# Kernel optimization log

Measured on AMD Instinct MI355X. Metric: run time of the kernel, lower is better.

Reference implementation:

```python
import jax, jax.numpy as jnp
import numpy as np

V, N = 3, 32768
C2, C3 = 256, 32          # feat_ch_2D, feat_ch_3D
H = W = 128               # 2D feature map size
D = 32                    # 3D volume feature size
CIN = C2 + C3             # 288, MLP in_channels


def setup_inputs() -> dict:
    key = jax.random.key(0)
    ks = jax.random.split(key, 16)
    sc = 0.02
    inp = {
        'pts': jax.random.uniform(ks[0], (1, N, 3), minval=-0.5, maxval=0.5),
        'pts_proj': jax.random.uniform(ks[1], (1, N, 2), minval=-1.0, maxval=1.0),
        'img_feat0': jax.random.normal(ks[2], (V, C2, H, W)),
        'img_feat1': jax.random.normal(ks[3], (V, C2, H, W)),
        'vol_feat0': jax.random.normal(ks[4], (V, C3, D, D, D)),
        'vol_feat1': jax.random.normal(ks[5], (V, C3, D, D, D)),
        'W0': jax.random.normal(ks[6], (1024, CIN)) * sc,  'b0': jnp.zeros((1024,)),
        'W1': jax.random.normal(ks[7], (512, CIN + 1024)) * sc, 'b1': jnp.zeros((512,)),
        'W2': jax.random.normal(ks[8], (256, CIN + 512)) * sc,  'b2': jnp.zeros((256,)),
        'W3': jax.random.normal(ks[9], (128, CIN + 256)) * sc,  'b3': jnp.zeros((128,)),
        'W4': jax.random.normal(ks[10], (1, 128)) * sc,         'b4': jnp.zeros((1,)),
        'mean_num': 3,
    }
    return inp


def _gs2d(feat, gx, gy):
    # feat: [C,H,W]; gx,gy: [N] normalized coords in [-1,1]
    C, Hh, Ww = feat.shape
    ix = jnp.clip(((gx + 1.0) * Ww - 1.0) * 0.5, 0.0, Ww - 1.0)  # align_corners=False, border pad
    iy = jnp.clip(((gy + 1.0) * Hh - 1.0) * 0.5, 0.0, Hh - 1.0)
    x0f, y0f = jnp.floor(ix), jnp.floor(iy)
    wx, wy = ix - x0f, iy - y0f
    x0 = x0f.astype(jnp.int32); x1 = jnp.minimum(x0 + 1, Ww - 1)
    y0 = y0f.astype(jnp.int32); y1 = jnp.minimum(y0 + 1, Hh - 1)
    v00 = feat[:, y0, x0]; v01 = feat[:, y0, x1]
    v10 = feat[:, y1, x0]; v11 = feat[:, y1, x1]
    return (v00 * (1 - wy) * (1 - wx) + v01 * (1 - wy) * wx
            + v10 * wy * (1 - wx) + v11 * wy * wx)  # [C,N]


def _gs3d(feat, gx, gy, gz):
    # feat: [C,D,H,W]; grid x->W, y->H, z->D (torch grid_sample convention)
    C, Dd, Hh, Ww = feat.shape
    ix = jnp.clip(((gx + 1.0) * Ww - 1.0) * 0.5, 0.0, Ww - 1.0)
    iy = jnp.clip(((gy + 1.0) * Hh - 1.0) * 0.5, 0.0, Hh - 1.0)
    iz = jnp.clip(((gz + 1.0) * Dd - 1.0) * 0.5, 0.0, Dd - 1.0)
    x0f, y0f, z0f = jnp.floor(ix), jnp.floor(iy), jnp.floor(iz)
    wx, wy, wz = ix - x0f, iy - y0f, iz - z0f
    x0 = x0f.astype(jnp.int32); x1 = jnp.minimum(x0 + 1, Ww - 1)
    y0 = y0f.astype(jnp.int32); y1 = jnp.minimum(y0 + 1, Hh - 1)
    z0 = z0f.astype(jnp.int32); z1 = jnp.minimum(z0 + 1, Dd - 1)
    def g(zi, yi, xi):
        return feat[:, zi, yi, xi]  # [C,N]
    out = (g(z0, y0, x0) * (1 - wz) * (1 - wy) * (1 - wx)
           + g(z0, y0, x1) * (1 - wz) * (1 - wy) * wx
           + g(z0, y1, x0) * (1 - wz) * wy * (1 - wx)
           + g(z0, y1, x1) * (1 - wz) * wy * wx
           + g(z1, y0, x0) * wz * (1 - wy) * (1 - wx)
           + g(z1, y0, x1) * wz * (1 - wy) * wx
           + g(z1, y1, x0) * wz * wy * (1 - wx)
           + g(z1, y1, x1) * wz * wy * wx)
    return out  # [C,N]


def _lrelu(x):
    return jnp.where(x >= 0, x, 0.2 * x)


def _conv1x1(Wm, bm, x):
    # x: [V,C,N] -> [V,O,N]
    return jnp.einsum('oc,vcn->von', Wm, x) + bm[None, :, None]


def _mlp0(x, W0, b0, W1, b1, W2, b2, W3, b3):
    out = _lrelu(_conv1x1(W0, b0, x))
    out = _lrelu(_conv1x1(W1, b1, jnp.concatenate([x, out], axis=1)))
    out = _lrelu(_conv1x1(W2, b2, jnp.concatenate([x, out], axis=1)))
    out = _lrelu(_conv1x1(W3, b3, jnp.concatenate([x, out], axis=1)))
    return out  # [V,128,N]


def _forward(pts, pts_proj, img_feats, vol_feats,
             W0, b0, W1, b1, W2, b2, W3, b3, W4, b4, mean_num):
    v = img_feats[0].shape[0]
    gx2 = jnp.broadcast_to(pts_proj[:, :, 0], (v, pts_proj.shape[1]))
    gy2 = jnp.broadcast_to(pts_proj[:, :, 1], (v, pts_proj.shape[1]))
    p = pts * 2.0  # pts *= 2.0 before 3D sampling
    gx3 = jnp.broadcast_to(p[:, :, 0], (v, p.shape[1]))
    gy3 = jnp.broadcast_to(p[:, :, 1], (v, p.shape[1]))
    gz3 = jnp.broadcast_to(p[:, :, 2], (v, p.shape[1]))
    outs = []
    for img_feat, vol_feat in zip(img_feats, vol_feats):
        f2 = jax.vmap(_gs2d)(img_feat, gx2, gy2)            # [V,C2,N]
        f3 = jax.vmap(_gs3d)(vol_feat, gx3, gy3, gz3)       # [V,C3,N]
        pt_feat = jnp.concatenate([f2, f3], axis=1)         # [V,288,N]
        pt_out0 = _mlp0(pt_feat, W0, b0, W1, b1, W2, b2, W3, b3)
        pt_out0_mean = jnp.mean(pt_out0[:mean_num], axis=0, keepdims=True)  # [1,128,N]
        sdf = jax.nn.sigmoid(_conv1x1(W4, b4, pt_out0_mean))                # [1,1,N]
        outs.append(jnp.transpose(sdf, (0, 2, 1)))                          # [1,N,1]
    return tuple(outs)


def reference(pts, pts_proj, img_feat0, img_feat1, vol_feat0, vol_feat1,
              W0, b0, W1, b1, W2, b2, W3, b3, W4, b4, mean_num):
    return _forward(pts, pts_proj, [img_feat0, img_feat1], [vol_feat0, vol_feat1],
                    W0, b0, W1, b1, W2, b2, W3, b3, W4, b4, mean_num)
```

## Files before the change

### kernel.cpp

```cpp
#include <hip/hip_runtime.h>
#include <hip/hip_bf16.h>

#define NV 3
#define NPTS 32768
#define C2C 256
#define C3C 32
#define CINC 288
#define CINP 320
#define HH 128
#define WWW 128
#define DDD 32

typedef short bh8 __attribute__((ext_vector_type(8)));
typedef float fx4 __attribute__((ext_vector_type(4)));
typedef unsigned short us4 __attribute__((ext_vector_type(4)));

__device__ __forceinline__ float b2f(unsigned short u) {
    unsigned int x = ((unsigned int)u) << 16;
    return __uint_as_float(x);
}
__device__ __forceinline__ unsigned short f2b(float f) {
    unsigned int x = __float_as_uint(f);
    unsigned int r = (x + 0x7FFFu + ((x >> 16) & 1u)) >> 16;
    return (unsigned short)r;
}

__device__ __forceinline__ void gl2lds16(const unsigned short* g, unsigned short* l) {
    __builtin_amdgcn_global_load_lds(
        (const __attribute__((address_space(1))) unsigned int*)g,
        (__attribute__((address_space(3))) unsigned int*)l, 16, 0, 0);
}

__device__ __forceinline__ int xcd_swz(int orig, int nwg) {
    int xcd = orig & 7;
    int q = nwg >> 3, r = nwg & 7;
    int base = (xcd < r) ? xcd * (q + 1) : r * (q + 1) + (xcd - r) * q;
    return base + (orig >> 3);
}

__global__ void k_wpad(const float* __restrict__ src, unsigned short* __restrict__ dst, int M, int Kp) {
    int idx = blockIdx.x * 256 + threadIdx.x;
    if (idx >= M * Kp) return;
    int m = idx / Kp, k = idx - m * Kp;
    int Ksrc = Kp - 32;
    float v;
    if (k < CINC) v = src[(size_t)m * Ksrc + k];
    else if (k < CINP) v = 0.0f;
    else v = src[(size_t)m * Ksrc + (k - 32)];
    dst[idx] = f2b(v);
}

__global__ void k_timg(const float* __restrict__ in, unsigned short* __restrict__ out) {
    int v = blockIdx.x >> 7, y = blockIdx.x & 127;
    int x0 = blockIdx.y << 6, c0 = blockIdx.z << 6;
    __shared__ float t[64][65];
    int tx = threadIdx.x & 63, tg = threadIdx.x >> 6;
    const float* src = in + (((size_t)(v * C2C + c0) * HH + y) * WWW + x0);
#pragma unroll
    for (int i = 0; i < 16; i++) {
        int cl = tg * 16 + i;
        t[cl][tx] = src[(size_t)cl * (HH * WWW) + tx];
    }
    __syncthreads();
    unsigned short* dst = out + ((size_t)(v * HH + y) * WWW + x0) * C2C + c0;
#pragma unroll
    for (int i = 0; i < 16; i++) {
        int xl = tg * 16 + i;
        dst[(size_t)xl * C2C + tx] = f2b(t[tx][xl]);
    }
}

__global__ void k_tvol(const float* __restrict__ in, unsigned short* __restrict__ out) {
    int v = blockIdx.x;
    int s0 = blockIdx.y << 8;
    __shared__ float t[32][257];
    int tid = threadIdx.x;
    const float* src = in + (size_t)v * C3C * 32768 + s0;
#pragma unroll
    for (int c = 0; c < 32; c++) t[c][tid] = src[(size_t)c * 32768 + tid];
    __syncthreads();
    unsigned short* dst = out + ((size_t)v * 32768 + s0) * C3C;
    int c = tid & 31, sb = tid >> 5;
#pragma unroll
    for (int j = 0; j < 32; j++) {
        int sl = j * 8 + sb;
        dst[(size_t)sl * C3C + c] = f2b(t[c][sl]);
    }
}

__global__ __launch_bounds__(256) void k_sample(const float* __restrict__ pts, const float* __restrict__ proj,
                         const unsigned short* __restrict__ imgT, const unsigned short* __restrict__ volT,
                         unsigned short* __restrict__ ptT, int n0, int Nk) {
    int w = threadIdx.x >> 6, l = threadIdx.x & 63;
    int i = blockIdx.x * 4 + w;
    int v = blockIdx.y;
    int n = n0 + i;
    unsigned short* dstRow = ptT + (size_t)(v * Nk + i) * CINP;

    {
        float gx = proj[n * 2 + 0], gy = proj[n * 2 + 1];
        float ix = fminf(fmaxf(((gx + 1.0f) * (float)WWW - 1.0f) * 0.5f, 0.0f), (float)(WWW - 1));
        float iy = fminf(fmaxf(((gy + 1.0f) * (float)HH - 1.0f) * 0.5f, 0.0f), (float)(HH - 1));
        float x0f = floorf(ix), y0f = floorf(iy);
        float wx = ix - x0f, wy = iy - y0f;
        int x0 = (int)x0f, y0 = (int)y0f;
        int x1 = min(x0 + 1, WWW - 1), y1 = min(y0 + 1, HH - 1);
        const unsigned short* base = imgT + (size_t)v * HH * WWW * C2C;
        us4 a = *((const us4*)(base + ((size_t)(y0 * WWW + x0)) * C2C) + l);
        us4 b = *((const us4*)(base + ((size_t)(y0 * WWW + x1)) * C2C) + l);
        us4 c = *((const us4*)(base + ((size_t)(y1 * WWW + x0)) * C2C) + l);
        us4 d = *((const us4*)(base + ((size_t)(y1 * WWW + x1)) * C2C) + l);
        float w00 = (1.0f - wy) * (1.0f - wx), w01 = (1.0f - wy) * wx;
        float w10 = wy * (1.0f - wx), w11 = wy * wx;
        us4 rv;
#pragma unroll
        for (int r = 0; r < 4; r++) {
            float f = b2f(a[r]) * w00 + b2f(b[r]) * w01 + b2f(c[r]) * w10 + b2f(d[r]) * w11;
            rv[r] = f2b(f);
        }
        *(us4*)(dstRow + l * 4) = rv;
    }
    {
        float gx = pts[n * 3 + 0] * 2.0f, gy = pts[n * 3 + 1] * 2.0f, gz = pts[n * 3 + 2] * 2.0f;
        float ix = fminf(fmaxf(((gx + 1.0f) * (float)DDD - 1.0f) * 0.5f, 0.0f), (float)(DDD - 1));
        float iy = fminf(fmaxf(((gy + 1.0f) * (float)DDD - 1.0f) * 0.5f, 0.0f), (float)(DDD - 1));
        float iz = fminf(fmaxf(((gz + 1.0f) * (float)DDD - 1.0f) * 0.5f, 0.0f), (float)(DDD - 1));
        float x0f = floorf(ix), y0f = floorf(iy), z0f = floorf(iz);
        float wx = ix - x0f, wy = iy - y0f, wz = iz - z0f;
        int x0 = (int)x0f, y0 = (int)y0f, z0 = (int)z0f;
        int x1 = min(x0 + 1, DDD - 1), y1 = min(y0 + 1, DDD - 1), z1 = min(z0 + 1, DDD - 1);
        int c = l & 31, zs = l >> 5;
        int zi = zs ? z1 : z0;
        float wzs = zs ? wz : (1.0f - wz);
        const unsigned short* base = volT + (size_t)v * 32768 * C3C;
        float f00 = b2f(base[((size_t)((zi * 32 + y0) * 32 + x0)) * C3C + c]);
        float f01 = b2f(base[((size_t)((zi * 32 + y0) * 32 + x1)) * C3C + c]);
        float f10 = b2f(base[((size_t)((zi * 32 + y1) * 32 + x0)) * C3C + c]);
        float f11 = b2f(base[((size_t)((zi * 32 + y1) * 32 + x1)) * C3C + c]);
        float r = (f00 * (1.0f - wy) * (1.0f - wx) + f01 * (1.0f - wy) * wx +
                   f10 * wy * (1.0f - wx) + f11 * wy * wx) * wzs;
        float other = __shfl_xor(r, 32);
        r += other;
        if (zs == 0) dstRow[C2C + c] = f2b(r);
    }
    if (l < 8) *(us4*)(dstRow + CINC + l * 4) = (us4){0, 0, 0, 0};
}

__global__ __launch_bounds__(512) void k_gemm8(const unsigned short* __restrict__ A, int Kp,
                                               const unsigned short* __restrict__ B1,
                                               const unsigned short* __restrict__ B2, int K2,
                                               const float* __restrict__ bias,
                                               unsigned short* __restrict__ C, int M) {
    __shared__ unsigned short As[2][256 * 64];
    __shared__ unsigned short Bs[2][256 * 64];
    int tid = threadIdx.x;
    int w = tid >> 6, l = tid & 63;
    int la = l & 15, lg = l >> 4;
    int wm = w >> 2, wn = w & 3;
    int g = wn >> 1;
    int gx = gridDim.x;
    int nwg = gx * gridDim.y;
    int bid = xcd_swz(blockIdx.y * gx + blockIdx.x, nwg);
    int mBlk = (bid % gx) * 256;
    int nBlk = (bid / gx) * 256;
    int nt = Kp >> 6;

    const unsigned short* Ag = A + (size_t)mBlk * Kp;

    fx4 acc[8][4];
#pragma unroll
    for (int mi = 0; mi < 8; mi++)
#pragma unroll
        for (int ni = 0; ni < 4; ni++) acc[mi][ni] = (fx4){0.f, 0.f, 0.f, 0.f};

    auto burst = [&](int t, int nxt) {
        const unsigned short* bsrc;
        size_t ldb;
        int kc;
        if (t < 5) { bsrc = B1; ldb = CINP; kc = t * 64; }
        else       { bsrc = B2; ldb = (size_t)K2; kc = (t - 5) * 64; }
        bsrc += (size_t)nBlk * ldb + kc;
        const unsigned short* asrc = Ag + t * 64;
#pragma unroll
        for (int h = 0; h < 2; h++)
#pragma unroll
            for (int j = 0; j < 2; j++) {
                int idx = j * 512 + tid;
                int r = (h << 7) + (idx >> 3);
                int c = (idx & 7) ^ (r & 7);
                gl2lds16(asrc + (size_t)r * Kp + c * 8, &As[nxt][(h << 13) + idx * 8]);
            }
#pragma unroll
        for (int h = 0; h < 2; h++)
#pragma unroll
            for (int j = 0; j < 2; j++) {
                int idx = j * 512 + tid;
                int r = (h << 7) + (idx >> 3);
                int c = (idx & 7) ^ (r & 7);
                gl2lds16(bsrc + (size_t)r * ldb + c * 8, &Bs[nxt][(h << 13) + idx * 8]);
            }
    };

    burst(0, 0);
    for (int t = 0; t < nt; t++) {
        int cur = t & 1;
        if (t + 1 < nt) {
            burst(t + 1, cur ^ 1);
            if (g == 0) asm volatile("s_waitcnt vmcnt(10)" ::: "memory");
            else        asm volatile("s_waitcnt vmcnt(8)" ::: "memory");
        } else {
            if (g == 0) asm volatile("s_waitcnt vmcnt(2)" ::: "memory");
            else        asm volatile("s_waitcnt vmcnt(0)" ::: "memory");
        }
        const unsigned short* Ab = &As[cur][0];
        const unsigned short* Bb = &Bs[cur][0];
        bh8 afr[4][2];
#pragma unroll
        for (int p = 0; p < 4; p++) {
            int qm = p >> 1, qn = p & 1;
            if (qn == 0) {
#pragma unroll
                for (int m2 = 0; m2 < 4; m2++)
#pragma unroll
                    for (int s = 0; s < 2; s++) {
                        int row = wm * 128 + (qm * 4 + m2) * 16 + la;
                        int c = (s * 4 + lg) ^ (row & 7);
                        afr[m2][s] = *(const bh8*)&Ab[row * 64 + c * 8];
                    }
            }
            bh8 bfr[2][2];
#pragma unroll
            for (int n2 = 0; n2 < 2; n2++)
#pragma unroll
                for (int s = 0; s < 2; s++) {
                    int row = wn * 64 + (qn * 2 + n2) * 16 + la;
                    int c = (s * 4 + lg) ^ (row & 7);
                    bfr[n2][s] = *(const bh8*)&Bb[row * 64 + c * 8];
                }
            __builtin_amdgcn_s_barrier();
            __builtin_amdgcn_s_setprio(1);
#pragma unroll
            for (int m2 = 0; m2 < 4; m2++)
#pragma unroll
                for (int n2 = 0; n2 < 2; n2++)
#pragma unroll
                    for (int s = 0; s < 2; s++)
                        acc[qm * 4 + m2][qn * 2 + n2] = __builtin_amdgcn_mfma_f32_16x16x32_bf16(
                            afr[m2][s], bfr[n2][s], acc[qm * 4 + m2][qn * 2 + n2], 0, 0, 0);
            __builtin_amdgcn_s_setprio(0);
            if (p == 3) asm volatile("s_waitcnt lgkmcnt(0)" ::: "memory");
            __builtin_amdgcn_s_barrier();
        }
    }

#pragma unroll
    for (int mi = 0; mi < 8; mi++) {
        int m0 = mBlk + wm * 128 + mi * 16 + lg * 4;
        fx4 bb = *(const fx4*)(bias + m0);
#pragma unroll
        for (int ni = 0; ni < 4; ni++) {
            int n = nBlk + wn * 64 + ni * 16 + la;
            us4 rv;
#pragma unroll
            for (int r = 0; r < 4; r++) {
                float x = acc[mi][ni][r] + bb[r];
                x = (x >= 0.0f) ? x : 0.2f * x;
                rv[r] = f2b(x);
            }
            *(us4*)(C + (size_t)n * M + m0) = rv;
        }
    }
}

__global__ __launch_bounds__(256) void k_gemm(const unsigned short* __restrict__ A, int K,
                                              const unsigned short* __restrict__ B1, int K1,
                                              const unsigned short* __restrict__ B2, int K2,
                                              const float* __restrict__ bias,
                                              unsigned short* __restrict__ C, int M) {
    __shared__ unsigned short Ash[128 * 32];
    __shared__ unsigned short Bsh[128 * 32];
    int tid = threadIdx.x;
    int w = tid >> 6, l = tid & 63;
    int la = l & 15, lg = l >> 4;
    int wm = w & 1, wn = w >> 1;
    int gx = gridDim.x;
    int nwg = gx * gridDim.y;
    int bid = xcd_swz(blockIdx.y * gx + blockIdx.x, nwg);
    int mBlk = (bid % gx) * 128;
    int nBlk = (bid / gx) * 128;

    int sRow = l >> 2;
    int sCol = (l & 3) * 8;

    fx4 acc[4][4];
#pragma unroll
    for (int mi = 0; mi < 4; mi++)
#pragma unroll
        for (int ni = 0; ni < 4; ni++) acc[mi][ni] = (fx4){0.f, 0.f, 0.f, 0.f};

    const unsigned short* Ag = A + (size_t)mBlk * K;
    const unsigned short* Bg;

#define KLOOP(BPTR, KB, AOFF)                                                                  \
    Bg = (BPTR) + (size_t)nBlk * (KB);                                                         \
    for (int k0 = 0; k0 < (KB); k0 += 32) {                                                    \
        _Pragma("unroll")                                                                      \
        for (int j = 0; j < 2; j++) {                                                          \
            int r = w * 32 + j * 16 + sRow;                                                    \
            gl2lds16(Ag + (size_t)r * K + (AOFF) + k0 + sCol, &Ash[r * 32 + sCol]);            \
            gl2lds16(Bg + (size_t)r * (KB) + k0 + sCol, &Bsh[r * 32 + sCol]);                  \
        }                                                                                      \
        __syncthreads();                                                                       \
        bh8 af[4], bfv[4];                                                                     \
        _Pragma("unroll")                                                                      \
        for (int mi = 0; mi < 4; mi++) af[mi] = *(const bh8*)&Ash[(wm * 64 + mi * 16 + la) * 32 + lg * 8]; \
        _Pragma("unroll")                                                                      \
        for (int ni = 0; ni < 4; ni++) bfv[ni] = *(const bh8*)&Bsh[(wn * 64 + ni * 16 + la) * 32 + lg * 8]; \
        _Pragma("unroll")                                                                      \
        for (int mi = 0; mi < 4; mi++)                                                         \
            _Pragma("unroll")                                                                  \
            for (int ni = 0; ni < 4; ni++)                                                     \
                acc[mi][ni] = __builtin_amdgcn_mfma_f32_16x16x32_bf16(af[mi], bfv[ni], acc[mi][ni], 0, 0, 0); \
        __syncthreads();                                                                       \
    }

    KLOOP(B1, K1, 0)
    if (B2 != nullptr) {
        KLOOP(B2, K2, K1)
    }
#undef KLOOP

#pragma unroll
    for (int mi = 0; mi < 4; mi++) {
        int m0 = mBlk + wm * 64 + mi * 16 + lg * 4;
        fx4 bb = *(const fx4*)(bias + m0);
#pragma unroll
        for (int ni = 0; ni < 4; ni++) {
            int n = nBlk + wn * 64 + ni * 16 + la;
            us4 rv;
#pragma unroll
            for (int r = 0; r < 4; r++) {
                float x = acc[mi][ni][r] + bb[r];
                x = (x >= 0.0f) ? x : 0.2f * x;
                rv[r] = f2b(x);
            }
            *(us4*)(C + (size_t)n * M + m0) = rv;
        }
    }
}

__global__ void k_head(const unsigned short* __restrict__ o3, const float* __restrict__ W4,
                       const float* __restrict__ b4, const int* __restrict__ mn_p,
                       float* __restrict__ out, int n0, int Nk, int level) {
    int i = blockIdx.x * 256 + threadIdx.x;
    if (i >= Nk) return;
    int mn = *mn_p;
    if (mn > NV) mn = NV;
    if (mn < 1) mn = 1;
    float s = 0.0f;
    for (int v = 0; v < mn; v++) {
        const unsigned short* row = o3 + (size_t)(v * Nk + i) * 128;
        for (int c0 = 0; c0 < 128; c0 += 8) {
            bh8 x = *(const bh8*)(row + c0);
#pragma unroll
            for (int r = 0; r < 8; r++) s += W4[c0 + r] * b2f((unsigned short)x[r]);
        }
    }
    s = s / (float)mn + b4[0];
    out[(size_t)level * NPTS + n0 + i] = 1.0f / (1.0f + expf(-s));
}

extern "C" void kernel_launch(void* const* d_in, const int* in_sizes, int n_in,
                              void* d_out, int out_size, void* d_ws, size_t ws_size,
                              hipStream_t stream) {
    const float* pts = (const float*)d_in[0];
    const float* proj = (const float*)d_in[1];
    const float* img[2] = {(const float*)d_in[2], (const float*)d_in[3]};
    const float* vol[2] = {(const float*)d_in[4], (const float*)d_in[5]};
    const float* Wf[4] = {(const float*)d_in[6], (const float*)d_in[8], (const float*)d_in[10], (const float*)d_in[12]};
    const float* bf[4] = {(const float*)d_in[7], (const float*)d_in[9], (const float*)d_in[11], (const float*)d_in[13]};
    const float* W4 = (const float*)d_in[14];
    const float* b4 = (const float*)d_in[15];
    const int* mn = (const int*)d_in[16];
    float* out = (float*)d_out;

    const int Kp[4] = {320, 1344, 832, 576};
    const int Msz[4] = {1024, 512, 256, 128};

    char* ws = (char*)d_ws;
    size_t off = 0;
    auto alloc = [&](size_t bytes) -> char* {
        char* p = ws + off;
        off = (off + bytes + 255) & ~(size_t)255;
        return p;
    };

    unsigned short* Wb[4];
    for (int i = 0; i < 4; i++) Wb[i] = (unsigned short*)alloc((size_t)Msz[i] * Kp[i] * 2);
    unsigned short* imgT = (unsigned short*)alloc((size_t)NV * HH * WWW * C2C * 2);
    unsigned short* volT = (unsigned short*)alloc((size_t)NV * 32768 * C3C * 2);
    size_t fixed = off;

    const size_t perPt = (size_t)NV * 2 * (CINP + 1024 + 512 + 256 + 128);
    int Nk = NPTS;
    if (fixed + (size_t)Nk * perPt + 4096 > ws_size) {
        size_t avail = (ws_size > fixed + 4096) ? (ws_size - fixed - 4096) : 0;
        long nk = (long)(avail / perPt);
        nk = (nk / 256) * 256;
        if (nk < 256) nk = 256;
        if (nk > NPTS) nk = NPTS;
        Nk = (int)nk;
    }
    unsigned short* ptT = (unsigned short*)alloc((size_t)NV * Nk * CINP * 2);
    unsigned short* o0 = (unsigned short*)alloc((size_t)NV * Nk * 1024 * 2);
    unsigned short* o1 = (unsigned short*)alloc((size_t)NV * Nk * 512 * 2);
    unsigned short* o2 = (unsigned short*)alloc((size_t)NV * Nk * 256 * 2);
    unsigned short* o3 = (unsigned short*)alloc((size_t)NV * Nk * 128 * 2);

    for (int i = 0; i < 4; i++) {
        int n = Msz[i] * Kp[i];
        k_wpad<<<(n + 255) / 256, 256, 0, stream>>>(Wf[i], Wb[i], Msz[i], Kp[i]);
    }

    for (int lvl = 0; lvl < 2; lvl++) {
        k_timg<<<dim3(NV * HH, WWW / 64, C2C / 64), 256, 0, stream>>>(img[lvl], imgT);
        k_tvol<<<dim3(NV, 32768 / 256), 256, 0, stream>>>(vol[lvl], volT);
        for (int n0 = 0; n0 < NPTS; n0 += Nk) {
            int nk = NPTS - n0 < Nk ? NPTS - n0 : Nk;
            int NC = NV * nk;
            k_sample<<<dim3(nk / 4, NV), 256, 0, stream>>>(pts, proj, imgT, volT, ptT, n0, nk);
            k_gemm8<<<dim3(1024 / 256, NC / 256), 512, 0, stream>>>(Wb[0], Kp[0], ptT, nullptr, 0, bf[0], o0, 1024);
            k_gemm8<<<dim3(512 / 256, NC / 256), 512, 0, stream>>>(Wb[1], Kp[1], ptT, o0, 1024, bf[1], o1, 512);
            k_gemm8<<<dim3(256 / 256, NC / 256), 512, 0, stream>>>(Wb[2], Kp[2], ptT, o1, 512, bf[2], o2, 256);
            k_gemm<<<dim3(128 / 128, NC / 128), 256, 0, stream>>>(Wb[3], Kp[3], ptT, CINP, o2, 256, bf[3], o3, 128);
            k_head<<<(nk + 255) / 256, 256, 0, stream>>>(o3, W4, b4, mn, out, n0, nk, lvl);
        }
    }
}
```

Measured before the change: 1.183 ms.

## Batch both feature levels into a single MLP pass and switch layer tile kernels

Transposes both levels' image and volume features up front, then samples and runs the MLP for both levels at once. Each GEMM launch therefore covers twice as many columns, which halves the number of launches and gives more blocks per grid. Layers 0 and 2 also move from the 256-tile k_gemm8 kernel to the 128-tile k_gemm kernel. The cost is double the workspace for activations and a smaller per-chunk point count if the workspace is tight.

Result: slower. 1.233 ms (+4.3%).

```diff
diff --git a/kernel.cpp b/kernel.cpp
--- a/kernel.cpp
+++ b/kernel.cpp
@@ -90,12 +90,14 @@
 
 __global__ __launch_bounds__(256) void k_sample(const float* __restrict__ pts, const float* __restrict__ proj,
                          const unsigned short* __restrict__ imgT, const unsigned short* __restrict__ volT,
+                         size_t imgStride, size_t volStride,
                          unsigned short* __restrict__ ptT, int n0, int Nk) {
     int w = threadIdx.x >> 6, l = threadIdx.x & 63;
     int i = blockIdx.x * 4 + w;
     int v = blockIdx.y;
+    int lvl = blockIdx.z;
     int n = n0 + i;
-    unsigned short* dstRow = ptT + (size_t)(v * Nk + i) * CINP;
+    unsigned short* dstRow = ptT + (size_t)((lvl * NV + v) * Nk + i) * CINP;
 
     {
         float gx = proj[n * 2 + 0], gy = proj[n * 2 + 1];
@@ -105,7 +107,7 @@
         float wx = ix - x0f, wy = iy - y0f;
         int x0 = (int)x0f, y0 = (int)y0f;
         int x1 = min(x0 + 1, WWW - 1), y1 = min(y0 + 1, HH - 1);
-        const unsigned short* base = imgT + (size_t)v * HH * WWW * C2C;
+        const unsigned short* base = imgT + lvl * imgStride + (size_t)v * HH * WWW * C2C;
         us4 a = *((const us4*)(base + ((size_t)(y0 * WWW + x0)) * C2C) + l);
         us4 b = *((const us4*)(base + ((size_t)(y0 * WWW + x1)) * C2C) + l);
         us4 c = *((const us4*)(base + ((size_t)(y1 * WWW + x0)) * C2C) + l);
@@ -132,7 +134,7 @@
         int c = l & 31, zs = l >> 5;
         int zi = zs ? z1 : z0;
         float wzs = zs ? wz : (1.0f - wz);
-        const unsigned short* base = volT + (size_t)v * 32768 * C3C;
+        const unsigned short* base = volT + lvl * volStride + (size_t)v * 32768 * C3C;
         float f00 = b2f(base[((size_t)((zi * 32 + y0) * 32 + x0)) * C3C + c]);
         float f01 = b2f(base[((size_t)((zi * 32 + y0) * 32 + x1)) * C3C + c]);
         float f10 = b2f(base[((size_t)((zi * 32 + y1) * 32 + x0)) * C3C + c]);
@@ -351,15 +353,16 @@
 
 __global__ void k_head(const unsigned short* __restrict__ o3, const float* __restrict__ W4,
                        const float* __restrict__ b4, const int* __restrict__ mn_p,
-                       float* __restrict__ out, int n0, int Nk, int level) {
+                       float* __restrict__ out, int n0, int Nk) {
     int i = blockIdx.x * 256 + threadIdx.x;
+    int lvl = blockIdx.y;
     if (i >= Nk) return;
     int mn = *mn_p;
     if (mn > NV) mn = NV;
     if (mn < 1) mn = 1;
     float s = 0.0f;
     for (int v = 0; v < mn; v++) {
-        const unsigned short* row = o3 + (size_t)(v * Nk + i) * 128;
+        const unsigned short* row = o3 + (size_t)((lvl * NV + v) * Nk + i) * 128;
         for (int c0 = 0; c0 < 128; c0 += 8) {
             bh8 x = *(const bh8*)(row + c0);
 #pragma unroll
@@ -367,7 +370,7 @@
         }
     }
     s = s / (float)mn + b4[0];
-    out[(size_t)level * NPTS + n0 + i] = 1.0f / (1.0f + expf(-s));
+    out[(size_t)lvl * NPTS + n0 + i] = 1.0f / (1.0f + expf(-s));
 }
 
 extern "C" void kernel_launch(void* const* d_in, const int* in_sizes, int n_in,
@@ -395,45 +398,48 @@
         return p;
     };
 
+    const size_t imgStride = (size_t)NV * HH * WWW * C2C;
+    const size_t volStride = (size_t)NV * 32768 * C3C;
+
     unsigned short* Wb[4];
     for (int i = 0; i < 4; i++) Wb[i] = (unsigned short*)alloc((size_t)Msz[i] * Kp[i] * 2);
-    unsigned short* imgT = (unsigned short*)alloc((size_t)NV * HH * WWW * C2C * 2);
-    unsigned short* volT = (unsigned short*)alloc((size_t)NV * 32768 * C3C * 2);
+    unsigned short* imgT = (unsigned short*)alloc(2 * imgStride * 2);
+    unsigned short* volT = (unsigned short*)alloc(2 * volStride * 2);
     size_t fixed = off;
 
-    const size_t perPt = (size_t)NV * 2 * (CINP + 1024 + 512 + 256 + 128);
+    const size_t perPt = (size_t)2 * NV * 2 * (CINP + 1024 + 512 + 256 + 128);
     int Nk = NPTS;
     if (fixed + (size_t)Nk * perPt + 4096 > ws_size) {
         size_t avail = (ws_size > fixed + 4096) ? (ws_size - fixed - 4096) : 0;
         long nk = (long)(avail / perPt);
-        nk = (nk / 256) * 256;
-        if (nk < 256) nk = 256;
+        nk = (nk / 128) * 128;
+        if (nk < 128) nk = 128;
         if (nk > NPTS) nk = NPTS;
         Nk = (int)nk;
     }
-    unsigned short* ptT = (unsigned short*)alloc((size_t)NV * Nk * CINP * 2);
-    unsigned short* o0 = (unsigned short*)alloc((size_t)NV * Nk * 1024 * 2);
-    unsigned short* o1 = (unsigned short*)alloc((size_t)NV * Nk * 512 * 2);
-    unsigned short* o2 = (unsigned short*)alloc((size_t)NV * Nk * 256 * 2);
-    unsigned short* o3 = (unsigned short*)alloc((size_t)NV * Nk * 128 * 2);
+    unsigned short* ptT = (unsigned short*)alloc((size_t)2 * NV * Nk * CINP * 2);
+    unsigned short* o0 = (unsigned short*)alloc((size_t)2 * NV * Nk * 1024 * 2);
+    unsigned short* o1 = (unsigned short*)alloc((size_t)2 * NV * Nk * 512 * 2);
+    unsigned short* o2 = (unsigned short*)alloc((size_t)2 * NV * Nk * 256 * 2);
+    unsigned short* o3 = (unsigned short*)alloc((size_t)2 * NV * Nk * 128 * 2);
 
     for (int i = 0; i < 4; i++) {
         int n = Msz[i] * Kp[i];
         k_wpad<<<(n + 255) / 256, 256, 0, stream>>>(Wf[i], Wb[i], Msz[i], Kp[i]);
     }
-
     for (int lvl = 0; lvl < 2; lvl++) {
-        k_timg<<<dim3(NV * HH, WWW / 64, C2C / 64), 256, 0, stream>>>(img[lvl], imgT);
-        k_tvol<<<dim3(NV, 32768 / 256), 256, 0, stream>>>(vol[lvl], volT);
-        for (int n0 = 0; n0 < NPTS; n0 += Nk) {
-            int nk = NPTS - n0 < Nk ? NPTS - n0 : Nk;
-            int NC = NV * nk;
-            k_sample<<<dim3(nk / 4, NV), 256, 0, stream>>>(pts, proj, imgT, volT, ptT, n0, nk);
-            k_gemm8<<<dim3(1024 / 256, NC / 256), 512, 0, stream>>>(Wb[0], Kp[0], ptT, nullptr, 0, bf[0], o0, 1024);
-            k_gemm8<<<dim3(512 / 256, NC / 256), 512, 0, stream>>>(Wb[1], Kp[1], ptT, o0, 1024, bf[1], o1, 512);
-            k_gemm8<<<dim3(256 / 256, NC / 256), 512, 0, stream>>>(Wb[2], Kp[2], ptT, o1, 512, bf[2], o2, 256);
-            k_gemm<<<dim3(128 / 128, NC / 128), 256, 0, stream>>>(Wb[3], Kp[3], ptT, CINP, o2, 256, bf[3], o3, 128);
-            k_head<<<(nk + 255) / 256, 256, 0, stream>>>(o3, W4, b4, mn, out, n0, nk, lvl);
-        }
-    }
-}
+        k_timg<<<dim3(NV * HH, WWW / 64, C2C / 64), 256, 0, stream>>>(img[lvl], imgT + lvl * imgStride);
+        k_tvol<<<dim3(NV, 32768 / 256), 256, 0, stream>>>(vol[lvl], volT + lvl * volStride);
+    }
+
+    for (int n0 = 0; n0 < NPTS; n0 += Nk) {
+        int nk = NPTS - n0 < Nk ? NPTS - n0 : Nk;
+        int NC = 2 * NV * nk;
+        k_sample<<<dim3(nk / 4, NV, 2), 256, 0, stream>>>(pts, proj, imgT, volT, imgStride, volStride, ptT, n0, nk);
+        k_gemm<<<dim3(1024 / 128, NC / 128), 256, 0, stream>>>(Wb[0], Kp[0], ptT, CINP, nullptr, 0, bf[0], o0, 1024);
+        k_gemm8<<<dim3(512 / 256, NC / 256), 512, 0, stream>>>(Wb[1], Kp[1], ptT, o0, 1024, bf[1], o1, 512);
+        k_gemm<<<dim3(256 / 128, NC / 128), 256, 0, stream>>>(Wb[2], Kp[2], ptT, CINP, o1, 512, bf[2], o2, 256);
+        k_gemm<<<dim3(128 / 128, NC / 128), 256, 0, stream>>>(Wb[3], Kp[3], ptT, CINP, o2, 256, bf[3], o3, 128);
+        k_head<<<dim3((nk + 255) / 256, 2), 256, 0, stream>>>(o3, W4, b4, mn, out, n0, nk);
+    }
+}
```

## Specialize GEMM kernels per layer with compile-time shapes and smaller tiles

Applied to the files above, without the earlier changes.

Replaces the generic 256x256 k_gemm8 for layers 0 and 2 with a templated 128x128 single-buffered GEMM body that has K and M fixed at compile time. Layer 1 keeps the large double-buffered kernel, now with constant K and M. The smaller tiles give more workgroups for the narrow layers, and the constants let the compiler unroll loops and fold address math. The cost is less data reuse per tile and no LDS double buffering for layers 0 and 2.

Result: faster. 1.079 ms (-8.8%).

```diff
diff --git a/kernel.cpp b/kernel.cpp
--- a/kernel.cpp
+++ b/kernel.cpp
@@ -146,11 +146,125 @@
     if (l < 8) *(us4*)(dstRow + CINC + l * 4) = (us4){0, 0, 0, 0};
 }
 
-__global__ __launch_bounds__(512) void k_gemm8(const unsigned short* __restrict__ A, int Kp,
-                                               const unsigned short* __restrict__ B1,
-                                               const unsigned short* __restrict__ B2, int K2,
-                                               const float* __restrict__ bias,
-                                               unsigned short* __restrict__ C, int M) {
+template <int K1, int K2, int M>
+__device__ __forceinline__ void gemm128_body(const unsigned short* __restrict__ A,
+                                             const unsigned short* __restrict__ B1,
+                                             const unsigned short* __restrict__ B2,
+                                             const float* __restrict__ bias,
+                                             unsigned short* __restrict__ C) {
+    constexpr int K = K1 + K2;
+    __shared__ unsigned short Ash[128 * 32];
+    __shared__ unsigned short Bsh[128 * 32];
+    int tid = threadIdx.x;
+    int w = tid >> 6, l = tid & 63;
+    int la = l & 15, lg = l >> 4;
+    int wm = w & 1, wn = w >> 1;
+    int gx = gridDim.x;
+    int nwg = gx * gridDim.y;
+    int bid = xcd_swz(blockIdx.y * gx + blockIdx.x, nwg);
+    int mBlk = (bid % gx) * 128;
+    int nBlk = (bid / gx) * 128;
+
+    int sRow = l >> 2;
+    int sCol = (l & 3) * 8;
+
+    fx4 acc[4][4];
+#pragma unroll
+    for (int mi = 0; mi < 4; mi++)
+#pragma unroll
+        for (int ni = 0; ni < 4; ni++) acc[mi][ni] = (fx4){0.f, 0.f, 0.f, 0.f};
+
+    const unsigned short* Ag = A + (size_t)mBlk * K;
+    {
+        const unsigned short* Bg = B1 + (size_t)nBlk * K1;
+        for (int k0 = 0; k0 < K1; k0 += 32) {
+#pragma unroll
+            for (int j = 0; j < 2; j++) {
+                int r = w * 32 + j * 16 + sRow;
+                gl2lds16(Ag + (size_t)r * K + k0 + sCol, &Ash[r * 32 + sCol]);
+                gl2lds16(Bg + (size_t)r * K1 + k0 + sCol, &Bsh[r * 32 + sCol]);
+            }
+            __syncthreads();
+            bh8 af[4], bfv[4];
+#pragma unroll
+            for (int mi = 0; mi < 4; mi++) af[mi] = *(const bh8*)&Ash[(wm * 64 + mi * 16 + la) * 32 + lg * 8];
+#pragma unroll
+            for (int ni = 0; ni < 4; ni++) bfv[ni] = *(const bh8*)&Bsh[(wn * 64 + ni * 16 + la) * 32 + lg * 8];
+#pragma unroll
+            for (int mi = 0; mi < 4; mi++)
+#pragma unroll
+                for (int ni = 0; ni < 4; ni++)
+                    acc[mi][ni] = __builtin_amdgcn_mfma_f32_16x16x32_bf16(af[mi], bfv[ni], acc[mi][ni], 0, 0, 0);
+            __syncthreads();
+        }
+    }
+    if constexpr (K2 > 0) {
+        const unsigned short* Bg = B2 + (size_t)nBlk * K2;
+        for (int k0 = 0; k0 < K2; k0 += 32) {
+#pragma unroll
+            for (int j = 0; j < 2; j++) {
+                int r = w * 32 + j * 16 + sRow;
+                gl2lds16(Ag + (size_t)r * K + K1 + k0 + sCol, &Ash[r * 32 + sCol]);
+                gl2lds16(Bg + (size_t)r * K2 + k0 + sCol, &Bsh[r * 32 + sCol]);
+            }
+            __syncthreads();
+            bh8 af[4], bfv[4];
+#pragma unroll
+            for (int mi = 0; mi < 4; mi++) af[mi] = *(const bh8*)&Ash[(wm * 64 + mi * 16 + la) * 32 + lg * 8];
+#pragma unroll
+            for (int ni = 0; ni < 4; ni++) bfv[ni] = *(const bh8*)&Bsh[(wn * 64 + ni * 16 + la) * 32 + lg * 8];
+#pragma unroll
+            for (int mi = 0; mi < 4; mi++)
+#pragma unroll
+                for (int ni = 0; ni < 4; ni++)
+                    acc[mi][ni] = __builtin_amdgcn_mfma_f32_16x16x32_bf16(af[mi], bfv[ni], acc[mi][ni], 0, 0, 0);
+            __syncthreads();
+        }
+    }
+
+#pragma unroll
+    for (int mi = 0; mi < 4; mi++) {
+        int m0 = mBlk + wm * 64 + mi * 16 + lg * 4;
+        fx4 bb = *(const fx4*)(bias + m0);
+#pragma unroll
+        for (int ni = 0; ni < 4; ni++) {
+            int n = nBlk + wn * 64 + ni * 16 + la;
+            us4 rv;
+#pragma unroll
+            for (int r = 0; r < 4; r++) {
+                float x = acc[mi][ni][r] + bb[r];
+                x = (x >= 0.0f) ? x : 0.2f * x;
+                rv[r] = f2b(x);
+            }
+            *(us4*)(C + (size_t)n * M + m0) = rv;
+        }
+    }
+}
+
+__global__ __launch_bounds__(256) void k_g0(const unsigned short* __restrict__ A, const unsigned short* __restrict__ B1,
+                                            const float* __restrict__ bias, unsigned short* __restrict__ C) {
+    gemm128_body<320, 0, 1024>(A, B1, nullptr, bias, C);
+}
+__global__ __launch_bounds__(256) void k_g2(const unsigned short* __restrict__ A, const unsigned short* __restrict__ B1,
+                                            const unsigned short* __restrict__ B2, const float* __restrict__ bias,
+                                            unsigned short* __restrict__ C) {
+    gemm128_body<320, 512, 256>(A, B1, B2, bias, C);
+}
+__global__ __launch_bounds__(256) void k_g3(const unsigned short* __restrict__ A, const unsigned short* __restrict__ B1,
+                                            const unsigned short* __restrict__ B2, const float* __restrict__ bias,
+                                            unsigned short* __restrict__ C) {
+    gemm128_body<320, 256, 128>(A, B1, B2, bias, C);
+}
+
+__global__ __launch_bounds__(512) void k_g1(const unsigned short* __restrict__ A,
+                                            const unsigned short* __restrict__ B1,
+                                            const unsigned short* __restrict__ B2,
+                                            const float* __restrict__ bias,
+                                            unsigned short* __restrict__ C) {
+    constexpr int Kp = 1344;
+    constexpr int K2 = 1024;
+    constexpr int M = 512;
+    constexpr int nt = Kp >> 6;
     __shared__ unsigned short As[2][256 * 64];
     __shared__ unsigned short Bs[2][256 * 64];
     int tid = threadIdx.x;
@@ -163,7 +277,6 @@
     int bid = xcd_swz(blockIdx.y * gx + blockIdx.x, nwg);
     int mBlk = (bid % gx) * 256;
     int nBlk = (bid / gx) * 256;
-    int nt = Kp >> 6;
 
     const unsigned short* Ag = A + (size_t)mBlk * Kp;
 
@@ -256,83 +369,6 @@
 #pragma unroll
     for (int mi = 0; mi < 8; mi++) {
         int m0 = mBlk + wm * 128 + mi * 16 + lg * 4;
-        fx4 bb = *(const fx4*)(bias + m0);
-#pragma unroll
-        for (int ni = 0; ni < 4; ni++) {
-            int n = nBlk + wn * 64 + ni * 16 + la;
-            us4 rv;
-#pragma unroll
-            for (int r = 0; r < 4; r++) {
-                float x = acc[mi][ni][r] + bb[r];
-                x = (x >= 0.0f) ? x : 0.2f * x;
-                rv[r] = f2b(x);
-            }
-            *(us4*)(C + (size_t)n * M + m0) = rv;
-        }
-    }
-}
-
-__global__ __launch_bounds__(256) void k_gemm(const unsigned short* __restrict__ A, int K,
-                                              const unsigned short* __restrict__ B1, int K1,
-                                              const unsigned short* __restrict__ B2, int K2,
-                                              const float* __restrict__ bias,
-                                              unsigned short* __restrict__ C, int M) {
-    __shared__ unsigned short Ash[128 * 32];
-    __shared__ unsigned short Bsh[128 * 32];
-    int tid = threadIdx.x;
-    int w = tid >> 6, l = tid & 63;
-    int la = l & 15, lg = l >> 4;
-    int wm = w & 1, wn = w >> 1;
-    int gx = gridDim.x;
-    int nwg = gx * gridDim.y;
-    int bid = xcd_swz(blockIdx.y * gx + blockIdx.x, nwg);
-    int mBlk = (bid % gx) * 128;
-    int nBlk = (bid / gx) * 128;
-
-    int sRow = l >> 2;
-    int sCol = (l & 3) * 8;
-
-    fx4 acc[4][4];
-#pragma unroll
-    for (int mi = 0; mi < 4; mi++)
-#pragma unroll
-        for (int ni = 0; ni < 4; ni++) acc[mi][ni] = (fx4){0.f, 0.f, 0.f, 0.f};
-
-    const unsigned short* Ag = A + (size_t)mBlk * K;
-    const unsigned short* Bg;
-
-#define KLOOP(BPTR, KB, AOFF)                                                                  \
-    Bg = (BPTR) + (size_t)nBlk * (KB);                                                         \
-    for (int k0 = 0; k0 < (KB); k0 += 32) {                                                    \
-        _Pragma("unroll")                                                                      \
-        for (int j = 0; j < 2; j++) {                                                          \
-            int r = w * 32 + j * 16 + sRow;                                                    \
-            gl2lds16(Ag + (size_t)r * K + (AOFF) + k0 + sCol, &Ash[r * 32 + sCol]);            \
-            gl2lds16(Bg + (size_t)r * (KB) + k0 + sCol, &Bsh[r * 32 + sCol]);                  \
-        }                                                                                      \
-        __syncthreads();                                                                       \
-        bh8 af[4], bfv[4];                                                                     \
-        _Pragma("unroll")                                                                      \
-        for (int mi = 0; mi < 4; mi++) af[mi] = *(const bh8*)&Ash[(wm * 64 + mi * 16 + la) * 32 + lg * 8]; \
-        _Pragma("unroll")                                                                      \
-        for (int ni = 0; ni < 4; ni++) bfv[ni] = *(const bh8*)&Bsh[(wn * 64 + ni * 16 + la) * 32 + lg * 8]; \
-        _Pragma("unroll")                                                                      \
-        for (int mi = 0; mi < 4; mi++)                                                         \
-            _Pragma("unroll")                                                                  \
-            for (int ni = 0; ni < 4; ni++)                                                     \
-                acc[mi][ni] = __builtin_amdgcn_mfma_f32_16x16x32_bf16(af[mi], bfv[ni], acc[mi][ni], 0, 0, 0); \
-        __syncthreads();                                                                       \
-    }
-
-    KLOOP(B1, K1, 0)
-    if (B2 != nullptr) {
-        KLOOP(B2, K2, K1)
-    }
-#undef KLOOP
-
-#pragma unroll
-    for (int mi = 0; mi < 4; mi++) {
-        int m0 = mBlk + wm * 64 + mi * 16 + lg * 4;
         fx4 bb = *(const fx4*)(bias + m0);
 #pragma unroll
         for (int ni = 0; ni < 4; ni++) {
@@ -429,10 +465,10 @@
             int nk = NPTS - n0 < Nk ? NPTS - n0 : Nk;
             int NC = NV * nk;
             k_sample<<<dim3(nk / 4, NV), 256, 0, stream>>>(pts, proj, imgT, volT, ptT, n0, nk);
-            k_gemm8<<<dim3(1024 / 256, NC / 256), 512, 0, stream>>>(Wb[0], Kp[0], ptT, nullptr, 0, bf[0], o0, 1024);
-            k_gemm8<<<dim3(512 / 256, NC / 256), 512, 0, stream>>>(Wb[1], Kp[1], ptT, o0, 1024, bf[1], o1, 512);
-            k_gemm8<<<dim3(256 / 256, NC / 256), 512, 0, stream>>>(Wb[2], Kp[2], ptT, o1, 512, bf[2], o2, 256);
-            k_gemm<<<dim3(128 / 128, NC / 128), 256, 0, stream>>>(Wb[3], Kp[3], ptT, CINP, o2, 256, bf[3], o3, 128);
+            k_g0<<<dim3(1024 / 128, NC / 128), 256, 0, stream>>>(Wb[0], ptT, bf[0], o0);
+            k_g1<<<dim3(512 / 256, NC / 256), 512, 0, stream>>>(Wb[1], ptT, o0, bf[1], o1);
+            k_g2<<<dim3(256 / 128, NC / 128), 256, 0, stream>>>(Wb[2], ptT, o1, bf[2], o2);
+            k_g3<<<dim3(128 / 128, NC / 128), 256, 0, stream>>>(Wb[3], ptT, o2, bf[3], o3);
             k_head<<<(nk + 255) / 256, 256, 0, stream>>>(o3, W4, b4, mn, out, n0, nk, lvl);
         }
     }
```
